# Performance work log

Measured on AMD Instinct MI355X. Metric: run time of the kernel, lower is better.

Reference implementation:

```python
import jax, jax.numpy as jnp
import numpy as np
from jax import lax

B, N, CIN, COUT, FPS, K, TCH, M, H = 8, 4096, 128, 256, 1024, 24, 256, 32, 4
HD = TCH // H
BN_SCALE = 1.0 / np.sqrt(1.0 + 1e-5)  # eval-mode BN: running_mean=0, running_var=1


def _gather(points, idx):
    # points [B,N,C], idx [B,S] or [B,S,K] -> gathered points
    return jax.vmap(lambda p, i: p[i])(points, idx)


def _bn(x, g, b):
    return x * (g * BN_SCALE) + b


def _ln(x, g, b):
    mu = jnp.mean(x, -1, keepdims=True)
    v = jnp.var(x, -1, keepdims=True)
    return (x - mu) / jnp.sqrt(v + 1e-5) * g + b


def _gelu(x):
    return jax.nn.gelu(x, approximate=False)


def _fps(xyz, npoint, farthest0):
    Bb, Nn, _ = xyz.shape
    def step(carry, _):
        dmin, far = carry
        c = jax.vmap(lambda p, i: p[i])(xyz, far)  # [B,3]
        d = jnp.sum((xyz - c[:, None, :]) ** 2, -1)
        dmin = jnp.minimum(dmin, d)
        return (dmin, jnp.argmax(dmin, -1)), far
    init = (jnp.full((Bb, Nn), 1e10, xyz.dtype), farthest0)
    _, cents = lax.scan(step, init, None, length=npoint)
    return cents.T  # [B, npoint]


def _sqdist(src, dst):
    d = -2.0 * jnp.einsum('bnc,bmc->bnm', src, dst)
    d = d + jnp.sum(src ** 2, -1)[:, :, None]
    d = d + jnp.sum(dst ** 2, -1)[:, None, :]
    return d


def _forward(xyz, x, t, farthest0, Wproj, gproj, bproj, Wl1, gl1, bl1, Wl2, gl2, bl2,
             Wc1, gc1, bc1, Wc2, gc2, bc2, Wq, Wk, Wv, Wo,
             ln1g, ln1b, Wqkv, Wao, ln2g, ln2b, Wf1, Wf2):
    # --- GenerateGraph: FPS + KNN grouping ---
    fps_idx = _fps(xyz, FPS, farthest0)            # [B,S]
    new_xyz = _gather(xyz, fps_idx)                # [B,S,3]
    xT = jnp.transpose(x, (0, 2, 1))               # [B,N,Cin]
    new_pts = _gather(xT, fps_idx)                 # [B,S,Cin]
    dist = _sqdist(new_xyz, xyz)                   # [B,S,N]
    _, idx = lax.top_k(-dist, K)                   # [B,S,K] nearest neighbors
    grouped = _gather(xT, idx)                     # [B,S,K,Cin]
    edge = grouped - new_pts[:, :, None, :]
    # --- Local: Conv1DBR proj + Conv1DBRRes (channels-last, 1x1 convs = GEMM) ---
    h = _gelu(_bn(jnp.einsum('bskc,oc->bsko', edge, Wproj), gproj, bproj))
    r = _gelu(_bn(jnp.einsum('bsko,po->bskp', h, Wl1), gl1, bl1))
    r = _bn(jnp.einsum('bskp,op->bsko', r, Wl2), gl2, bl2)
    h = _gelu(r + h)
    f = jnp.max(h, axis=2)                         # adaptive_max_pool over k -> [B,S,O]
    # --- Channel (ca): Conv1DBRRes on centroid features ---
    r = _gelu(_bn(f @ Wc1.T, gc1, bc1))
    r = _bn(r @ Wc2.T, gc2, bc2)
    f = _gelu(r + f)
    x_out = jnp.transpose(f, (0, 2, 1))            # [B,O,S]
    # --- Local2Former: tokens attend to local features ---
    q = t @ Wq.T
    kk = f @ Wk.T
    v = f @ Wv.T
    a = jax.nn.softmax(jnp.einsum('bmd,bsd->bms', q, kk) * (TCH ** -0.5), axis=-1)
    t = t + jnp.einsum('bms,bsd->bmd', a, v) @ Wo.T
    # --- Former: one pre-norm encoder layer (MHA + MLP) ---
    hn = _ln(t, ln1g, ln1b)
    qkv = (hn @ Wqkv.T).reshape(B, M, 3, H, HD).transpose(2, 0, 3, 1, 4)
    qh, kh, vh = qkv[0], qkv[1], qkv[2]            # [B,H,M,hd]
    attn = jax.nn.softmax(jnp.einsum('bhmd,bhnd->bhmn', qh, kh) * (HD ** -0.5), axis=-1)
    o = jnp.einsum('bhmn,bhnd->bhmd', attn, vh).transpose(0, 2, 1, 3).reshape(B, M, TCH)
    t = t + o @ Wao.T
    hn = _ln(t, ln2g, ln2b)
    t = t + _gelu(hn @ Wf1.T) @ Wf2.T
    return new_xyz, x_out, t


def setup_inputs() -> dict:
    key = jax.random.key(0)
    ks = jax.random.split(key, 40)
    def w(k, o, i):
        return jax.random.normal(k, (o, i), jnp.float32) / np.sqrt(i)
    def g(k, c):
        return 1.0 + 0.1 * jax.random.normal(k, (c,), jnp.float32)
    def bta(k, c):
        return 0.1 * jax.random.normal(k, (c,), jnp.float32)
    inp = {
        'xyz': jax.random.normal(ks[0], (B, N, 3), jnp.float32),
        'x': jax.random.normal(ks[1], (B, CIN, N), jnp.float32),
        't': jax.random.normal(ks[2], (B, M, TCH), jnp.float32),
        'farthest0': jax.random.randint(ks[3], (B,), 0, N),
        'Wproj': w(ks[4], COUT, CIN), 'gproj': g(ks[5], COUT), 'bproj': bta(ks[6], COUT),
        'Wl1': w(ks[7], COUT, COUT), 'gl1': g(ks[8], COUT), 'bl1': bta(ks[9], COUT),
        'Wl2': w(ks[10], COUT, COUT), 'gl2': g(ks[11], COUT), 'bl2': bta(ks[12], COUT),
        'Wc1': w(ks[13], COUT, COUT), 'gc1': g(ks[14], COUT), 'bc1': bta(ks[15], COUT),
        'Wc2': w(ks[16], COUT, COUT), 'gc2': g(ks[17], COUT), 'bc2': bta(ks[18], COUT),
        'Wq': w(ks[19], TCH, TCH), 'Wk': w(ks[20], TCH, COUT), 'Wv': w(ks[21], TCH, COUT),
        'Wo': w(ks[22], TCH, TCH),
        'ln1g': g(ks[23], TCH), 'ln1b': bta(ks[24], TCH),
        'Wqkv': w(ks[25], 3 * TCH, TCH), 'Wao': w(ks[26], TCH, TCH),
        'ln2g': g(ks[27], TCH), 'ln2b': bta(ks[28], TCH),
        'Wf1': w(ks[29], 2 * TCH, TCH), 'Wf2': w(ks[30], TCH, 2 * TCH),
    }
    return inp


def reference(xyz, x, t, farthest0, Wproj, gproj, bproj, Wl1, gl1, bl1, Wl2, gl2, bl2,
              Wc1, gc1, bc1, Wc2, gc2, bc2, Wq, Wk, Wv, Wo,
              ln1g, ln1b, Wqkv, Wao, ln2g, ln2b, Wf1, Wf2):
    return _forward(xyz, x, t, farthest0, Wproj, gproj, bproj, Wl1, gl1, bl1, Wl2, gl2, bl2,
                    Wc1, gc1, bc1, Wc2, gc2, bc2, Wq, Wk, Wv, Wo,
                    ln1g, ln1b, Wqkv, Wao, ln2g, ln2b, Wf1, Wf2)
```

## Files before the change

### kernel.cpp

```cpp
#include <hip/hip_runtime.h>
#include <math.h>

#define Bc 8
#define Nc 4096
#define CINc 128
#define COUTc 256
#define Sc 1024
#define Kc 24
#define TCHc 256
#define Mc 32
#define Hc 4
#define HDc 64
#define MBAT (Sc*Kc)

#define BN_SCALE_F 0.9999950000374997f

typedef __attribute__((ext_vector_type(8))) short bf16x8;
typedef __attribute__((ext_vector_type(4))) float f32x4;
typedef __attribute__((ext_vector_type(2))) float f32x2;

__device__ __forceinline__ float b2f(short s){
  unsigned int u = ((unsigned int)(unsigned short)s) << 16;
  union { unsigned int u; float f; } c; c.u = u; return c.f;
}
__device__ __forceinline__ short f2b(float f){
  union { unsigned int u; float f; } c; c.f = f;
  unsigned int u = c.u;
  unsigned int r = (u + 0x7fffu + ((u >> 16) & 1u)) >> 16;
  return (short)(r & 0xffffu);
}
__device__ __forceinline__ float gelu_f(float v){
  return 0.5f * v * (1.f + erff(v * 0.7071067811865475f));
}
__device__ __forceinline__ float rdval(const float* p){ return *p; }
__device__ __forceinline__ float rdval(const short* p){ return b2f(*p); }
__device__ __forceinline__ void wrval(float* p, float v){ *p = v; }
__device__ __forceinline__ void wrval(short* p, float v){ *p = f2b(v); }

__device__ __forceinline__ void gl_lds16(const short* g, short* l){
  __builtin_amdgcn_global_load_lds(
     (const __attribute__((address_space(1))) void*)g,
     (__attribute__((address_space(3))) void*)l, 16, 0, 0);
}

__device__ __forceinline__ void bar_lds(){
  asm volatile("s_waitcnt lgkmcnt(0)" ::: "memory");
  __builtin_amdgcn_s_barrier();
}

__device__ __forceinline__ f32x2 pk_add(f32x2 a, f32x2 b){
  f32x2 d; asm("v_pk_add_f32 %0, %1, %2" : "=v"(d) : "v"(a), "v"(b)); return d;
}
__device__ __forceinline__ f32x2 pk_mul(f32x2 a, f32x2 b){
  f32x2 d; asm("v_pk_mul_f32 %0, %1, %2" : "=v"(d) : "v"(a), "v"(b)); return d;
}

__device__ __forceinline__ double packkey(float d, unsigned tag){
  return __longlong_as_double((long long)(
    (((unsigned long long)(unsigned)__float_as_int(d)) << 32) | (unsigned long long)tag));
}

template<int CTRL>
__device__ __forceinline__ double dpp_mov_f64(double v){
  long long x = __double_as_longlong(v);
  int lo = (int)(unsigned)(x & 0xFFFFFFFFLL);
  int hi = (int)(unsigned)((unsigned long long)x >> 32);
  int plo = __builtin_amdgcn_update_dpp(lo, lo, CTRL, 0xF, 0xF, false);
  int phi = __builtin_amdgcn_update_dpp(hi, hi, CTRL, 0xF, 0xF, false);
  return __longlong_as_double((long long)(((unsigned long long)(unsigned)phi << 32)
                                          | (unsigned)plo));
}
template<int CTRL>
__device__ __forceinline__ double dpp_min_f64(double v){
  return fmin(v, dpp_mov_f64<CTRL>(v));
}
template<int CTRL>
__device__ __forceinline__ float dpp_max_f32(float v){
  int p = __builtin_amdgcn_update_dpp(__float_as_int(v), __float_as_int(v), CTRL, 0xF, 0xF, false);
  return fmaxf(v, __int_as_float(p));
}

#define PREP_FPS 8
#define PREP_TOTAL 256
#define NWORK 248

__global__ __launch_bounds__(512) void prep_kernel(
    const float* __restrict__ xyz, const int* __restrict__ far0, int* __restrict__ fps_idx,
    const float* __restrict__ x, short* __restrict__ xT,
    const float* __restrict__ Wproj, const float* __restrict__ Wl1, const float* __restrict__ Wl2,
    const float* __restrict__ Wc1, const float* __restrict__ Wc2,
    const float* __restrict__ Wk, const float* __restrict__ Wv,
    const float* __restrict__ Wq, const float* __restrict__ Wo,
    const float* __restrict__ Wqkv, const float* __restrict__ Wao,
    const float* __restrict__ Wf1, const float* __restrict__ Wf2,
    const float* __restrict__ t_in,
    short* __restrict__ wbf,
    int* __restrict__ knn_idx, float* __restrict__ out0){
  __shared__ __align__(16) char smemc[57728];
  int bid = blockIdx.x, tid = threadIdx.x;
  if(bid < PREP_FPS){
    int b = bid;
    float* sx = (float*)smemc;
    float* sy = sx + Nc;
    float* sz = sy + Nc;
    double* pwave = (double*)(smemc + 49152);
    const float* xb = xyz + (size_t)b*Nc*3;
    for(int i=tid; i<Nc; i+=512){
      const float* p = xb + i*3;
      sx[i]=p[0]; sy[i]=p[1]; sz[i]=p[2];
    }
    __syncthreads();
    int lane = tid & 63, wv = tid >> 6;
    int base = wv*512 + lane*8;
    f32x2 px2[4], py2[4], pz2[4];
    float dmn[8];
#pragma unroll
    for(int i=0;i<4;i++){
      px2[i] = (f32x2){ sx[base+2*i], sx[base+2*i+1] };
      py2[i] = (f32x2){ sy[base+2*i], sy[base+2*i+1] };
      pz2[i] = (f32x2){ sz[base+2*i], sz[base+2*i+1] };
      dmn[2*i] = 1e10f; dmn[2*i+1] = 1e10f;
    }
    int winner = far0[b] & (Nc-1);
    int* out = fps_idx + b*Sc;
    for(int it=0; it<Sc; it++){
      if(tid==0)
        __hip_atomic_store(&out[it], winner, __ATOMIC_RELAXED, __HIP_MEMORY_SCOPE_AGENT);
      float cx=sx[winner], cy=sy[winner], cz=sz[winner];
      f32x2 ncx = (f32x2){-cx,-cx}, ncy = (f32x2){-cy,-cy}, ncz = (f32x2){-cz,-cz};
      float vmax = -1.f;
#pragma unroll
      for(int i=0;i<4;i++){
        f32x2 dx = pk_add(px2[i], ncx);
        f32x2 dy = pk_add(py2[i], ncy);
        f32x2 dz = pk_add(pz2[i], ncz);
        f32x2 d  = pk_add(pk_add(pk_mul(dx,dx), pk_mul(dy,dy)), pk_mul(dz,dz));
        dmn[2*i]   = fminf(dmn[2*i],   d[0]);
        dmn[2*i+1] = fminf(dmn[2*i+1], d[1]);
        vmax = fmaxf(vmax, fmaxf(dmn[2*i], dmn[2*i+1]));
      }
      float wm = vmax;
      wm = dpp_max_f32<0x111>(wm);
      wm = dpp_max_f32<0x112>(wm);
      wm = dpp_max_f32<0x114>(wm);
      wm = dpp_max_f32<0x118>(wm);
      wm = dpp_max_f32<0x142>(wm);
      wm = dpp_max_f32<0x143>(wm);
      float smax = __int_as_float(__builtin_amdgcn_readlane(__float_as_int(wm), 63));
      int lj = 0;
#pragma unroll
      for(int j=7;j>=0;j--) if(dmn[j]==smax) lj = j;
      unsigned long long mk = __ballot(vmax == smax);
      int flane = __ffsll(mk) - 1;
      int ljw = __builtin_amdgcn_readlane(lj, flane);
      int widx = wv*512 + flane*8 + ljw;
      if(lane==0)
        pwave[(it&1)*8 + wv] = packkey(smax, (unsigned)((Nc-1) - widx));
      bar_lds();
      const double* pb = pwave + (it&1)*8;
      double kb = fmax(fmax(fmax(pb[0],pb[1]), fmax(pb[2],pb[3])),
                       fmax(fmax(pb[4],pb[5]), fmax(pb[6],pb[7])));
      winner = (Nc-1) - (int)(unsigned)(__double_as_longlong(kb) & 0xFFFFFFFFULL);
    }
  } else {
    int wid = bid - PREP_FPS;
    int b = wid / 31;
    int widb = wid % 31;
    short (*tile)[33] = (short(*)[33])smemc;
    for(int t = wid; t < 4096; t += NWORK){
      int bb = t >> 9;
      int rem = t & 511;
      int n0 = (rem & 127) * 32;
      int c0 = (rem >> 7) * 32;
      int tx = tid & 31, ty = tid >> 5;
      __syncthreads();
#pragma unroll
      for(int i=0;i<32;i+=16)
        tile[ty+i][tx] = f2b(x[((size_t)bb*CINc + (c0+ty+i))*Nc + n0+tx]);
      __syncthreads();
#pragma unroll
      for(int i=0;i<32;i+=16)
        xT[((size_t)bb*Nc + (n0+ty+i))*CINc + c0+tx] = tile[tx][ty+i];
    }
    {
      int gid = wid*512 + tid;
      const int stride = NWORK*512;
      short* p = wbf;
      for(int i=gid; i<COUTc*CINc; i+=stride) p[i] = f2b(Wproj[i]);
      p += COUTc*CINc;
      for(int i=gid; i<COUTc*COUTc; i+=stride) p[i] = f2b(Wl1[i]);
      p += COUTc*COUTc;
      for(int i=gid; i<COUTc*COUTc; i+=stride) p[i] = f2b(Wl2[i]);
      p += COUTc*COUTc;
      for(int i=gid; i<COUTc*COUTc; i+=stride) p[i] = f2b(Wc1[i]);
      p += COUTc*COUTc;
      for(int i=gid; i<COUTc*COUTc; i+=stride) p[i] = f2b(Wc2[i]);
      p += COUTc*COUTc;
      for(int i=gid; i<TCHc*COUTc; i+=stride) p[i] = f2b(Wk[i]);
      p += TCHc*COUTc;
      for(int i=gid; i<TCHc*COUTc; i+=stride) p[i] = f2b(Wv[i]);
      p += TCHc*COUTc;
      for(int i=gid; i<TCHc*TCHc; i+=stride) p[i] = f2b(Wq[i]);
      p += TCHc*TCHc;
      for(int i=gid; i<TCHc*TCHc; i+=stride) p[i] = f2b(Wo[i]);
      p += TCHc*TCHc;
      for(int i=gid; i<3*TCHc*TCHc; i+=stride) p[i] = f2b(Wqkv[i]);
      p += 3*TCHc*TCHc;
      for(int i=gid; i<TCHc*TCHc; i+=stride) p[i] = f2b(Wao[i]);
      p += TCHc*TCHc;
      for(int i=gid; i<2*TCHc*TCHc; i+=stride) p[i] = f2b(Wf1[i]);
      p += 2*TCHc*TCHc;
      for(int i=gid; i<2*TCHc*TCHc; i+=stride) p[i] = f2b(Wf2[i]);
      p += 2*TCHc*TCHc;
      for(int i=gid; i<Bc*Mc*TCHc; i+=stride) p[i] = f2b(t_in[i]);
    }
    int* s_qn = (int*)(smemc + 2112);
    double* pvd = (double*)(smemc + 2176);
    const float* xb = xyz + (size_t)b*Nc*3;
    float px[8], py[8], pz[8], db[8];
#pragma unroll
    for(int j=0;j<8;j++){
      int n = tid + 512*j;
      float xx=xb[n*3], yy=xb[n*3+1], zz=xb[n*3+2];
      px[j]=xx; py[j]=yy; pz[j]=zz;
      db[j] = __fadd_rn(__fadd_rn(__fmul_rn(xx,xx),__fmul_rn(yy,yy)),__fmul_rn(zz,zz));
    }
    __syncthreads();
    for(int s = widb; s < Sc; s += 31){
      if(tid==0){
        int qn;
        for(;;){
          qn = __hip_atomic_load(&fps_idx[b*Sc + s], __ATOMIC_RELAXED, __HIP_MEMORY_SCOPE_AGENT);
          if(qn >= 0) break;
          __builtin_amdgcn_s_sleep(8);
        }
        s_qn[0] = qn & (Nc-1);
      }
      bar_lds();
      int qn = s_qn[0];
      const float* q = xyz + ((size_t)b*Nc + qn)*3;
      float sxq = q[0], syq = q[1], szq = q[2];
      if(tid < 3) out0[((size_t)b*Sc + s)*3 + tid] = q[tid];
      float ss = __fadd_rn(__fadd_rn(__fmul_rn(sxq,sxq),__fmul_rn(syq,syq)),__fmul_rn(szq,szq));
      float dv[8];
#pragma unroll
      for(int j=0;j<8;j++){
        float e = __fmul_rn(sxq,px[j]);
        e = __fadd_rn(e, __fmul_rn(syq,py[j]));
        e = __fadd_rn(e, __fmul_rn(szq,pz[j]));
        dv[j] = __fadd_rn(__fadd_rn(__fmul_rn(-2.f,e), ss), db[j]);
      }
      int* ob = knn_idx + ((size_t)b*Sc + s)*Kc;
      for(int k=0;k<Kc;k++){
        double kk = packkey(fmaxf(dv[0],0.f), (unsigned)tid);
#pragma unroll
        for(int j=1;j<8;j++) kk = fmin(kk, packkey(fmaxf(dv[j],0.f), (unsigned)(tid + 512*j)));
        kk = dpp_min_f64<0x111>(kk);
        kk = dpp_min_f64<0x112>(kk);
        kk = dpp_min_f64<0x114>(kk);
        kk = dpp_min_f64<0x118>(kk);
        kk = dpp_min_f64<0x142>(kk);
        kk = dpp_min_f64<0x143>(kk);
        double* pb = pvd + (k&1)*8;
        if((tid&63)==63) pb[tid>>6] = kk;
        bar_lds();
        double w0 = fmin(fmin(fmin(pb[0],pb[1]),fmin(pb[2],pb[3])),
                         fmin(fmin(pb[4],pb[5]),fmin(pb[6],pb[7])));
        int win = (int)(unsigned)(__double_as_longlong(w0) & 0xFFFFFFFFULL);
        if(tid==0) ob[k] = win;
#pragma unroll
        for(int j=0;j<8;j++) if(tid + 512*j == win) dv[j] = 3.4e38f;
      }
    }
  }
}

template<int HAS_BN, int HAS_GELU, int HAS_RES, typename TRES>
__global__ __launch_bounds__(256) void gemm128(
    const short* __restrict__ A, const short* __restrict__ W,
    const float* __restrict__ g, const float* __restrict__ bias,
    const TRES* __restrict__ Res, short* __restrict__ Out,
    int Nn, int Kk){
  __shared__ short As[128*32];
  __shared__ short Bs[128*32];
  int bm = blockIdx.y*128, bn = blockIdx.x*128;
  int tid = threadIdx.x;
  int wave = tid>>6, lane = tid&63, quad = lane>>4, l16 = lane&15;
  int wr = (wave>>1)*64, wc = (wave&1)*64;
  f32x4 acc[4][4];
#pragma unroll
  for(int i=0;i<4;i++)
#pragma unroll
    for(int j=0;j<4;j++) acc[i][j] = (f32x4){0.f,0.f,0.f,0.f};
  int sr = tid>>2, scc = (tid&3)*8;
  const short* Ap = A + (size_t)(bm+sr)*Kk + scc;
  const short* Wp = W + (size_t)(bn+sr)*Kk + scc;
  for(int k0=0; k0<Kk; k0+=32){
    gl_lds16(Ap + k0,                    As + tid*8);
    gl_lds16(Ap + k0 + (size_t)64*Kk,    As + 2048 + tid*8);
    gl_lds16(Wp + k0,                    Bs + tid*8);
    gl_lds16(Wp + k0 + (size_t)64*Kk,    Bs + 2048 + tid*8);
    __syncthreads();
    bf16x8 af[4], bfr[4];
#pragma unroll
    for(int mt=0; mt<4; mt++) af[mt]  = *(const bf16x8*)&As[(wr+mt*16+l16)*32 + quad*8];
#pragma unroll
    for(int nt=0; nt<4; nt++) bfr[nt] = *(const bf16x8*)&Bs[(wc+nt*16+l16)*32 + quad*8];
#pragma unroll
    for(int mt=0; mt<4; mt++)
#pragma unroll
      for(int nt=0; nt<4; nt++)
        acc[mt][nt] = __builtin_amdgcn_mfma_f32_16x16x32_bf16(af[mt], bfr[nt], acc[mt][nt], 0, 0, 0);
    __syncthreads();
  }
#pragma unroll
  for(int nt=0; nt<4; nt++){
    int col = bn + wc + nt*16 + l16;
    float gs = 0.f, bs_ = 0.f;
    if(HAS_BN){ gs = g[col] * BN_SCALE_F; bs_ = bias[col]; }
#pragma unroll
    for(int mt=0; mt<4; mt++){
#pragma unroll
      for(int r2=0;r2<4;r2++){
        int row = bm + wr + mt*16 + quad*4 + r2;
        float v = acc[mt][nt][r2];
        if(HAS_BN) v = v*gs + bs_;
        if(HAS_RES) v += rdval(Res + (size_t)row*Nn + col);
        if(HAS_GELU) v = gelu_f(v);
        Out[(size_t)row*Nn + col] = f2b(v);
      }
    }
  }
}

__global__ __launch_bounds__(256) void proj128(
    const short* __restrict__ xT, const int* __restrict__ knn_idx, const int* __restrict__ fps_idx,
    const short* __restrict__ W, const float* __restrict__ g, const float* __restrict__ bias,
    short* __restrict__ Out, int R0){
  __shared__ short As[128*32];
  __shared__ short Bs[128*32];
  int bm = blockIdx.y*128, bn = blockIdx.x*128;
  int tid = threadIdx.x;
  int wave = tid>>6, lane = tid&63, quad = lane>>4, l16 = lane&15;
  int wr = (wave>>1)*64, wc = (wave&1)*64;
  f32x4 acc[4][4];
#pragma unroll
  for(int i=0;i<4;i++)
#pragma unroll
    for(int j=0;j<4;j++) acc[i][j] = (f32x4){0.f,0.f,0.f,0.f};
  int sr = tid>>2, scc = (tid&3)*8;
  int Rg0 = R0 + bm + sr, Rg1 = Rg0 + 64;
  int b0 = Rg0 / (Sc*Kc), b1 = Rg1 / (Sc*Kc);
  int nk0 = knn_idx[Rg0] & (Nc-1), nk1 = knn_idx[Rg1] & (Nc-1);
  int nc0 = fps_idx[Rg0 / Kc] & (Nc-1), nc1 = fps_idx[Rg1 / Kc] & (Nc-1);
  const short* pk0 = xT + ((size_t)b0*Nc + nk0)*CINc + scc;
  const short* pc0 = xT + ((size_t)b0*Nc + nc0)*CINc + scc;
  const short* pk1 = xT + ((size_t)b1*Nc + nk1)*CINc + scc;
  const short* pc1 = xT + ((size_t)b1*Nc + nc1)*CINc + scc;
  const short* Wp  = W + (size_t)(bn+sr)*CINc + scc;
  for(int k0=0; k0<CINc; k0+=32){
    gl_lds16(Wp + k0,                      Bs + tid*8);
    gl_lds16(Wp + k0 + (size_t)64*CINc,    Bs + 2048 + tid*8);
    bf16x8 vk = *(const bf16x8*)(pk0 + k0);
    bf16x8 vc = *(const bf16x8*)(pc0 + k0);
    bf16x8 e0, e1;
#pragma unroll
    for(int i=0;i<8;i++) e0[i] = f2b(__fsub_rn(b2f(vk[i]), b2f(vc[i])));
    vk = *(const bf16x8*)(pk1 + k0);
    vc = *(const bf16x8*)(pc1 + k0);
#pragma unroll
    for(int i=0;i<8;i++) e1[i] = f2b(__fsub_rn(b2f(vk[i]), b2f(vc[i])));
    *(bf16x8*)&As[tid*8] = e0;
    *(bf16x8*)&As[2048 + tid*8] = e1;
    __syncthreads();
    bf16x8 af[4], bfr[4];
#pragma unroll
    for(int mt=0; mt<4; mt++) af[mt]  = *(const bf16x8*)&As[(wr+mt*16+l16)*32 + quad*8];
#pragma unroll
    for(int nt=0; nt<4; nt++) bfr[nt] = *(const bf16x8*)&Bs[(wc+nt*16+l16)*32 + quad*8];
#pragma unroll
    for(int mt=0; mt<4; mt++)
#pragma unroll
      for(int nt=0; nt<4; nt++)
        acc[mt][nt] = __builtin_amdgcn_mfma_f32_16x16x32_bf16(af[mt], bfr[nt], acc[mt][nt], 0, 0, 0);
    __syncthreads();
  }
#pragma unroll
  for(int nt=0; nt<4; nt++){
    int col = bn + wc + nt*16 + l16;
    float gs = g[col] * BN_SCALE_F, bs_ = bias[col];
#pragma unroll
    for(int mt=0; mt<4; mt++){
#pragma unroll
      for(int r2=0;r2<4;r2++){
        int row = bm + wr + mt*16 + quad*4 + r2;
        float v = acc[mt][nt][r2]*gs + bs_;
        Out[(size_t)row*COUTc + col] = f2b(gelu_f(v));
      }
    }
  }
}

__global__ __launch_bounds__(192) void gemm_l2max(
    const short* __restrict__ A, const short* __restrict__ W,
    const float* __restrict__ g, const float* __restrict__ bias,
    const short* __restrict__ Hres, short* __restrict__ Fout, int R0){
  __shared__ short As[48*32];
  __shared__ short Bs[64*32];
  __shared__ float sm[48][65];
  int bm = blockIdx.y*48, bn = blockIdx.x*64;
  int tid = threadIdx.x;
  int wave = tid >> 6, lane = tid & 63, quad = lane >> 4, l16 = lane & 15;
  f32x4 acc[4];
#pragma unroll
  for(int i=0;i<4;i++) acc[i] = (f32x4){0.f,0.f,0.f,0.f};
  const short* Ap  = A + (size_t)(bm + (tid>>2))*COUTc + (tid&3)*8;
  const short* Wp  = W + (size_t)(bn + (tid>>2))*COUTc + (tid&3)*8;
  const short* Wp2 = W + (size_t)(bn + 48 + (lane>>2))*COUTc + (lane&3)*8;
  for(int k0=0; k0<COUTc; k0+=32){
    gl_lds16(Ap + k0, As + tid*8);
    gl_lds16(Wp + k0, Bs + tid*8);
    if(wave==0) gl_lds16(Wp2 + k0, Bs + 1536 + lane*8);
    __syncthreads();
    bf16x8 a = *(const bf16x8*)&As[(wave*16 + l16)*32 + quad*8];
#pragma unroll
    for(int ct=0; ct<4; ct++){
      bf16x8 bb = *(const bf16x8*)&Bs[(ct*16 + l16)*32 + quad*8];
      acc[ct] = __builtin_amdgcn_mfma_f32_16x16x32_bf16(a, bb, acc[ct], 0, 0, 0);
    }
    __syncthreads();
  }
#pragma unroll
  for(int ct=0; ct<4; ct++){
    int col = bn + ct*16 + l16;
    float gs = g[col] * BN_SCALE_F, bs_ = bias[col];
#pragma unroll
    for(int r2=0;r2<4;r2++){
      int rl = wave*16 + quad*4 + r2;
      float v = acc[ct][r2]*gs + bs_;
      v += b2f(Hres[(size_t)(bm+rl)*COUTc + col]);
      sm[rl][ct*16 + l16] = gelu_f(v);
    }
  }
  __syncthreads();
  if(tid < 128){
    int gl = tid >> 6, col = tid & 63;
    float mx = -3.4e38f;
#pragma unroll
    for(int kk=0; kk<Kc; kk++) mx = fmaxf(mx, sm[gl*Kc + kk][col]);
    int gg = R0/Kc + blockIdx.y*2 + gl;
    Fout[(size_t)gg*COUTc + bn + col] = f2b(mx);
  }
}

template<int HAS_BN, int HAS_GELU, int HAS_RES, typename TRES, typename TOUT>
__global__ __launch_bounds__(256) void gemm64d(
    const short* __restrict__ A, const short* __restrict__ W,
    const float* __restrict__ g, const float* __restrict__ bias,
    const TRES* __restrict__ Res, TOUT* __restrict__ Out,
    int Nn, int Kk){
  __shared__ short As[64*32];
  __shared__ short Bs[64*32];
  int bm = blockIdx.y*64, bn = blockIdx.x*64;
  int tid = threadIdx.x;
  int wave = tid >> 6, lane = tid & 63, quad = lane >> 4, l16 = lane & 15;
  f32x4 acc[4];
#pragma unroll
  for(int i=0;i<4;i++) acc[i] = (f32x4){0.f,0.f,0.f,0.f};
  const short* Ap = A + (size_t)(bm + (tid>>2))*Kk + (tid&3)*8;
  const short* Wp = W + (size_t)(bn + (tid>>2))*Kk + (tid&3)*8;
  for(int k0=0; k0<Kk; k0+=32){
    gl_lds16(Ap + k0, As + tid*8);
    gl_lds16(Wp + k0, Bs + tid*8);
    __syncthreads();
    bf16x8 a = *(const bf16x8*)&As[(wave*16 + l16)*32 + quad*8];
#pragma unroll
    for(int ct=0; ct<4; ct++){
      bf16x8 bb = *(const bf16x8*)&Bs[(ct*16 + l16)*32 + quad*8];
      acc[ct] = __builtin_amdgcn_mfma_f32_16x16x32_bf16(a, bb, acc[ct], 0, 0, 0);
    }
    __syncthreads();
  }
#pragma unroll
  for(int ct=0; ct<4; ct++){
    int col = bn + ct*16 + l16;
    float gs = 0.f, bs_ = 0.f;
    if(HAS_BN){ gs = g[col] * BN_SCALE_F; bs_ = bias[col]; }
#pragma unroll
    for(int r2=0;r2<4;r2++){
      int row = bm + wave*16 + quad*4 + r2;
      float v = acc[ct][r2];
      if(HAS_BN) v = v*gs + bs_;
      if(HAS_RES) v += rdval(Res + (size_t)row*Nn + col);
      if(HAS_GELU) v = gelu_f(v);
      wrval(Out + (size_t)row*Nn + col, v);
    }
  }
}

__global__ __launch_bounds__(256) void transpose_f(const short* __restrict__ f2, float* __restrict__ out1){
  __shared__ short tile[32][33];
  int b = blockIdx.z;
  int s0 = blockIdx.x*32, c0 = blockIdx.y*32;
  int tx = threadIdx.x & 31, ty = threadIdx.x >> 5;
#pragma unroll
  for(int i=0;i<32;i+=8)
    tile[ty+i][tx] = f2[((size_t)b*Sc + (s0+ty+i))*COUTc + c0+tx];
  __syncthreads();
#pragma unroll
  for(int i=0;i<32;i+=8)
    out1[((size_t)b*COUTc + (c0+ty+i))*Sc + s0+tx] = b2f(tile[tx][ty+i]);
}

__global__ __launch_bounds__(256) void l2f_attn(
    const short* __restrict__ qb, const short* __restrict__ kv,
    short* __restrict__ ao){
  int blk = blockIdx.x; int b = blk / Mc; int m = blk % Mc;
  int tid = threadIdx.x;
  __shared__ float qs[TCHc];
  __shared__ float aw[Sc];
  __shared__ float red[8];
  qs[tid] = b2f(qb[(size_t)(b*Mc+m)*TCHc + tid]);
  __syncthreads();
  float sc[4];
#pragma unroll
  for(int jj=0;jj<4;jj++){
    int j = tid + 256*jj;
    const short* kp = kv + ((size_t)b*Sc + j)*512;
    float a = 0.f;
    for(int c=0;c<TCHc;c+=8){
      bf16x8 v8 = *(const bf16x8*)(kp + c);
#pragma unroll
      for(int i=0;i<8;i++) a += b2f(v8[i]) * qs[c+i];
    }
    sc[jj] = a * 0.0625f;
  }
  float mx = fmaxf(fmaxf(sc[0],sc[1]), fmaxf(sc[2],sc[3]));
#pragma unroll
  for(int off=32; off>0; off>>=1) mx = fmaxf(mx, __shfl_xor(mx, off));
  if((tid&63)==0) red[tid>>6] = mx;
  __syncthreads();
  mx = fmaxf(fmaxf(red[0],red[1]), fmaxf(red[2],red[3]));
  float se = 0.f;
#pragma unroll
  for(int jj=0;jj<4;jj++){
    float e = expf(sc[jj] - mx);
    aw[tid + 256*jj] = e;
    se += e;
  }
#pragma unroll
  for(int off=32; off>0; off>>=1) se += __shfl_xor(se, off);
  if((tid&63)==0) red[4 + (tid>>6)] = se;
  __syncthreads();
  se = red[4]+red[5]+red[6]+red[7];
  float inv = 1.f/se;
#pragma unroll
  for(int jj=0;jj<4;jj++) aw[tid + 256*jj] *= inv;
  __syncthreads();
  float acc = 0.f;
  const short* vp = kv + (size_t)b*Sc*512 + 256 + tid;
  for(int j=0;j<Sc;j++) acc += aw[j] * b2f(vp[(size_t)j*512]);
  ao[(size_t)(b*Mc+m)*TCHc + tid] = f2b(acc);
}

__global__ __launch_bounds__(64) void former_attn(const short* __restrict__ qkv, short* __restrict__ oa){
  int blk = blockIdx.x;
  int m = blk % Mc; int bh = blk / Mc; int h = bh % Hc; int b = bh / Hc;
  int lane = threadIdx.x;
  __shared__ float qs[HDc];
  __shared__ float aw2[32];
  const short* base = qkv + (size_t)(b*Mc)*(3*TCHc);
  qs[lane] = b2f(base[(size_t)m*3*TCHc + h*HDc + lane]);
  __syncthreads();
  int j = lane & 31;
  const short* kp = base + (size_t)j*3*TCHc + TCHc + h*HDc;
  float s = 0.f;
  for(int d=0; d<HDc; d+=8){
    bf16x8 v8 = *(const bf16x8*)(kp + d);
#pragma unroll
    for(int i=0;i<8;i++) s += b2f(v8[i]) * qs[d+i];
  }
  s *= 0.125f;
  float mx = s;
#pragma unroll
  for(int off=16; off>0; off>>=1) mx = fmaxf(mx, __shfl_xor(mx, off, 32));
  float e = expf(s - mx);
  float se = e;
#pragma unroll
  for(int off=16; off>0; off>>=1) se += __shfl_xor(se, off, 32);
  if(lane < 32) aw2[lane] = e / se;
  __syncthreads();
  float acc = 0.f;
  const short* vp = base + 2*TCHc + h*HDc + lane;
  for(int jj=0; jj<32; jj++) acc += aw2[jj] * b2f(vp[(size_t)jj*3*TCHc]);
  oa[(size_t)(b*Mc+m)*TCHc + h*HDc + lane] = f2b(acc);
}

__global__ __launch_bounds__(64) void ln_kernel(const float* __restrict__ X, const float* __restrict__ g,
                                                const float* __restrict__ bb, short* __restrict__ O){
  int row = blockIdx.x, lane = threadIdx.x;
  const float* xp = X + (size_t)row*TCHc;
  float x[4];
#pragma unroll
  for(int j2=0;j2<4;j2++) x[j2] = xp[lane + 64*j2];
  float sm = x[0]+x[1]+x[2]+x[3];
#pragma unroll
  for(int off=32; off>0; off>>=1) sm += __shfl_xor(sm, off);
  float mu = sm * (1.f/256.f);
  float vs = 0.f;
#pragma unroll
  for(int j2=0;j2<4;j2++){ float d = x[j2]-mu; vs += d*d; }
#pragma unroll
  for(int off=32; off>0; off>>=1) vs += __shfl_xor(vs, off);
  float var = vs * (1.f/256.f);
  float rstd = 1.f / sqrtf(var + 1e-5f);
#pragma unroll
  for(int j2=0;j2<4;j2++){
    int c = lane + 64*j2;
    float o = (x[j2]-mu)*rstd*g[c] + bb[c];
    O[(size_t)row*TCHc + c] = f2b(o);
  }
}

extern "C" void kernel_launch(void* const* d_in, const int* in_sizes, int n_in,
                              void* d_out, int out_size, void* d_ws, size_t ws_size,
                              hipStream_t stream){
  const float* xyz  = (const float*)d_in[0];
  const float* x    = (const float*)d_in[1];
  const float* t_in = (const float*)d_in[2];
  const int*   far0 = (const int*)d_in[3];
  const float* Wproj=(const float*)d_in[4];  const float* gproj=(const float*)d_in[5];  const float* bproj=(const float*)d_in[6];
  const float* Wl1 = (const float*)d_in[7];  const float* gl1 = (const float*)d_in[8];  const float* bl1 = (const float*)d_in[9];
  const float* Wl2 = (const float*)d_in[10]; const float* gl2 = (const float*)d_in[11]; const float* bl2 = (const float*)d_in[12];
  const float* Wc1 = (const float*)d_in[13]; const float* gc1 = (const float*)d_in[14]; const float* bc1 = (const float*)d_in[15];
  const float* Wc2 = (const float*)d_in[16]; const float* gc2 = (const float*)d_in[17]; const float* bc2 = (const float*)d_in[18];
  const float* Wq  = (const float*)d_in[19]; const float* Wk  = (const float*)d_in[20]; const float* Wv  = (const float*)d_in[21];
  const float* Wo  = (const float*)d_in[22];
  const float* ln1g= (const float*)d_in[23]; const float* ln1b= (const float*)d_in[24];
  const float* Wqkv= (const float*)d_in[25]; const float* Wao = (const float*)d_in[26];
  const float* ln2g= (const float*)d_in[27]; const float* ln2b= (const float*)d_in[28];
  const float* Wf1 = (const float*)d_in[29]; const float* Wf2 = (const float*)d_in[30];

  char* wsb = (char*)d_ws;
  size_t off = 0;
  auto alloc = [&](size_t bytes)->void*{ void* p = wsb + off; off += (bytes + 255) & ~(size_t)255; return p; };
  int*   fps_i = (int*)alloc((size_t)Bc*Sc*4);
  int*   knn   = (int*)alloc((size_t)Bc*Sc*Kc*4);
  short* xT    = (short*)alloc((size_t)Bc*Nc*CINc*2);
  size_t wbf_elems = (size_t)COUTc*CINc + 4*(size_t)COUTc*COUTc + 2*(size_t)TCHc*COUTc
                   + 2*(size_t)TCHc*TCHc + 3*(size_t)TCHc*TCHc + (size_t)TCHc*TCHc
                   + 2*(size_t)TCHc*TCHc + 2*(size_t)TCHc*TCHc + (size_t)Bc*Mc*TCHc;
  short* wbf   = (short*)alloc(wbf_elems*2);
  short* fbuf  = (short*)alloc((size_t)Bc*Sc*COUTc*2);
  short* rcbuf = (short*)alloc((size_t)Bc*Sc*COUTc*2);
  short* f2buf = (short*)alloc((size_t)Bc*Sc*COUTc*2);
  short* kvbuf = (short*)alloc((size_t)Bc*Sc*512*2);
  short* qbuf  = (short*)alloc((size_t)Bc*Mc*TCHc*2);
  short* a1out = (short*)alloc((size_t)Bc*Mc*TCHc*2);
  float* t1buf = (float*)alloc((size_t)Bc*Mc*TCHc*4);
  short* hnbuf = (short*)alloc((size_t)Bc*Mc*TCHc*2);
  short* qkvb  = (short*)alloc((size_t)Bc*Mc*3*TCHc*2);
  short* a2out = (short*)alloc((size_t)Bc*Mc*TCHc*2);
  float* t2buf = (float*)alloc((size_t)Bc*Mc*TCHc*4);
  short* hn2buf= (short*)alloc((size_t)Bc*Mc*TCHc*2);
  short* g1buf = (short*)alloc((size_t)Bc*Mc*2*TCHc*2);
  size_t full_bytes  = (size_t)Bc*MBAT*COUTc*2;
  size_t batch_bytes = (size_t)MBAT*COUTc*2;
  bool batched = (off + 2*(full_bytes + 256) <= ws_size);
  short* hbuf = (short*)alloc(batched ? full_bytes : batch_bytes);
  short* rbuf = (short*)alloc(batched ? full_bytes : batch_bytes);
  if(off > ws_size) return;

  short* wproj_bf = wbf;
  short* wl1_bf   = wproj_bf + COUTc*CINc;
  short* wl2_bf   = wl1_bf + COUTc*COUTc;
  short* wc1_bf   = wl2_bf + COUTc*COUTc;
  short* wc2_bf   = wc1_bf + COUTc*COUTc;
  short* wkv_bf   = wc2_bf + COUTc*COUTc;
  short* wq_bf    = wkv_bf + 2*TCHc*COUTc;
  short* wo_bf    = wq_bf + TCHc*TCHc;
  short* wqkv_bf  = wo_bf + TCHc*TCHc;
  short* wao_bf   = wqkv_bf + 3*TCHc*TCHc;
  short* wf1_bf   = wao_bf + TCHc*TCHc;
  short* wf2_bf   = wf1_bf + 2*TCHc*TCHc;
  short* tbf      = wf2_bf + 2*TCHc*TCHc;

  float* out0 = (float*)d_out;
  float* out1 = out0 + (size_t)Bc*Sc*3;
  float* out2 = out1 + (size_t)Bc*COUTc*Sc;

  hipMemsetAsync(fps_i, 0xFF, (size_t)Bc*Sc*4, stream);
  prep_kernel<<<PREP_TOTAL, 512, 0, stream>>>(xyz, far0, fps_i, x, xT,
                                              Wproj, Wl1, Wl2, Wc1, Wc2, Wk, Wv,
                                              Wq, Wo, Wqkv, Wao, Wf1, Wf2, t_in,
                                              wbf, knn, out0);
  if(batched){
    proj128<<<dim3(COUTc/128, (Bc*MBAT)/128), 256, 0, stream>>>(xT, knn, fps_i, wproj_bf, gproj, bproj, hbuf, 0);
    gemm128<1,1,0,short><<<dim3(COUTc/128, (Bc*MBAT)/128), 256, 0, stream>>>(hbuf, wl1_bf, gl1, bl1, (const short*)nullptr, rbuf, COUTc, COUTc);
    gemm_l2max<<<dim3(COUTc/64, (Bc*MBAT)/48), 192, 0, stream>>>(rbuf, wl2_bf, gl2, bl2, hbuf, fbuf, 0);
  } else {
    for(int b=0; b<Bc; b++){
      proj128<<<dim3(COUTc/128, MBAT/128), 256, 0, stream>>>(xT, knn, fps_i, wproj_bf, gproj, bproj, hbuf, b*MBAT);
      gemm128<1,1,0,short><<<dim3(COUTc/128, MBAT/128), 256, 0, stream>>>(hbuf, wl1_bf, gl1, bl1, (const short*)nullptr, rbuf, COUTc, COUTc);
      gemm_l2max<<<dim3(COUTc/64, MBAT/48), 192, 0, stream>>>(rbuf, wl2_bf, gl2, bl2, hbuf, fbuf, b*MBAT);
    }
  }
  gemm64d<1,1,0,short,short><<<dim3(COUTc/64, (Bc*Sc)/64), 256, 0, stream>>>(fbuf, wc1_bf, gc1, bc1, (const short*)nullptr, rcbuf, COUTc, COUTc);
  gemm64d<1,1,1,short,short><<<dim3(COUTc/64, (Bc*Sc)/64), 256, 0, stream>>>(rcbuf, wc2_bf, gc2, bc2, fbuf, f2buf, COUTc, COUTc);
  transpose_f<<<dim3(Sc/32, COUTc/32, Bc), 256, 0, stream>>>(f2buf, out1);
  gemm64d<0,0,0,short,short><<<dim3(TCHc/64, (Bc*Mc)/64), 256, 0, stream>>>(tbf, wq_bf, nullptr, nullptr, (const short*)nullptr, qbuf, TCHc, TCHc);
  gemm64d<0,0,0,short,short><<<dim3(512/64, (Bc*Sc)/64), 256, 0, stream>>>(f2buf, wkv_bf, nullptr, nullptr, (const short*)nullptr, kvbuf, 512, COUTc);
  l2f_attn<<<Bc*Mc, 256, 0, stream>>>(qbuf, kvbuf, a1out);
  gemm64d<0,0,1,float,float><<<dim3(TCHc/64, (Bc*Mc)/64), 256, 0, stream>>>(a1out, wo_bf, nullptr, nullptr, t_in, t1buf, TCHc, TCHc);
  ln_kernel<<<Bc*Mc, 64, 0, stream>>>(t1buf, ln1g, ln1b, hnbuf);
  gemm64d<0,0,0,short,short><<<dim3((3*TCHc)/64, (Bc*Mc)/64), 256, 0, stream>>>(hnbuf, wqkv_bf, nullptr, nullptr, (const short*)nullptr, qkvb, 3*TCHc, TCHc);
  former_attn<<<Bc*Hc*Mc, 64, 0, stream>>>(qkvb, a2out);
  gemm64d<0,0,1,float,float><<<dim3(TCHc/64, (Bc*Mc)/64), 256, 0, stream>>>(a2out, wao_bf, nullptr, nullptr, t1buf, t2buf, TCHc, TCHc);
  ln_kernel<<<Bc*Mc, 64, 0, stream>>>(t2buf, ln2g, ln2b, hn2buf);
  gemm64d<0,1,0,short,short><<<dim3((2*TCHc)/64, (Bc*Mc)/64), 256, 0, stream>>>(hn2buf, wf1_bf, nullptr, nullptr, (const short*)nullptr, g1buf, 2*TCHc, TCHc);
  gemm64d<0,0,1,float,float><<<dim3(TCHc/64, (Bc*Mc)/64), 256, 0, stream>>>(g1buf, wf2_bf, nullptr, nullptr, t2buf, out2, TCHc, 2*TCHc);
}
```

Before: 1.257 ms.

## Speculatively pick two FPS centroids per iteration using top-2 reduction

The farthest-point-sampling loop now reduces the top-2 packed (distance, index) keys per wave and across waves, instead of only the maximum. If the runner-up's distance to the new winner is at least its current min-distance, the runner-up must be the next FPS pick, so two centroids are emitted from one barrier round. This aims to roughly halve the serial block-barrier iterations on the FPS critical path. In exchange each reduction carries double-width keys and two DPP reduction chains, and the exactness relies on matching rounding in the recomputed distance check.

```diff
diff --git a/kernel.cpp b/kernel.cpp
--- a/kernel.cpp
+++ b/kernel.cpp
@@ -75,9 +75,14 @@
   return fmin(v, dpp_mov_f64<CTRL>(v));
 }
 template<int CTRL>
-__device__ __forceinline__ float dpp_max_f32(float v){
-  int p = __builtin_amdgcn_update_dpp(__float_as_int(v), __float_as_int(v), CTRL, 0xF, 0xF, false);
-  return fmaxf(v, __int_as_float(p));
+__device__ __forceinline__ double dpp_max_f64(double v){
+  return fmax(v, dpp_mov_f64<CTRL>(v));
+}
+__device__ __forceinline__ double readlane_f64(double v, int l){
+  long long x = __double_as_longlong(v);
+  int lo = __builtin_amdgcn_readlane((int)(unsigned)(x & 0xFFFFFFFFLL), l);
+  int hi = __builtin_amdgcn_readlane((int)(unsigned)((unsigned long long)x >> 32), l);
+  return __longlong_as_double((long long)(((unsigned long long)(unsigned)hi << 32) | (unsigned)lo));
 }
 
 #define PREP_FPS 8
@@ -103,7 +108,7 @@
     float* sx = (float*)smemc;
     float* sy = sx + Nc;
     float* sz = sy + Nc;
-    double* pwave = (double*)(smemc + 49152);
+    double* pw = (double*)(smemc + 49152);
     const float* xb = xyz + (size_t)b*Nc*3;
     for(int i=tid; i<Nc; i+=512){
       const float* p = xb + i*3;
@@ -113,54 +118,110 @@
     int lane = tid & 63, wv = tid >> 6;
     int base = wv*512 + lane*8;
     f32x2 px2[4], py2[4], pz2[4];
-    float dmn[8];
+    float dmn[8]; unsigned lokey[8];
 #pragma unroll
     for(int i=0;i<4;i++){
       px2[i] = (f32x2){ sx[base+2*i], sx[base+2*i+1] };
       py2[i] = (f32x2){ sy[base+2*i], sy[base+2*i+1] };
       pz2[i] = (f32x2){ sz[base+2*i], sz[base+2*i+1] };
       dmn[2*i] = 1e10f; dmn[2*i+1] = 1e10f;
-    }
-    int winner = far0[b] & (Nc-1);
+      lokey[2*i]   = (unsigned)((Nc-1) - (base+2*i));
+      lokey[2*i+1] = (unsigned)((Nc-1) - (base+2*i+1));
+    }
     int* out = fps_idx + b*Sc;
-    for(int it=0; it<Sc; it++){
+    int w0 = far0[b] & (Nc-1);
+    if(tid==0)
+      __hip_atomic_store(&out[0], w0, __ATOMIC_RELAXED, __HIP_MEMORY_SCOPE_AGENT);
+    float c1x = sx[w0], c1y = sy[w0], c1z = sz[w0];
+    float c2x = 0.f, c2y = 0.f, c2z = 0.f;
+    bool two = false;
+    int it = 1, fr = 0;
+    while(it < Sc){
+      if(two){
+        f32x2 n1x={-c1x,-c1x}, n1y={-c1y,-c1y}, n1z={-c1z,-c1z};
+        f32x2 n2x={-c2x,-c2x}, n2y={-c2y,-c2y}, n2z={-c2z,-c2z};
+#pragma unroll
+        for(int i=0;i<4;i++){
+          f32x2 dx=pk_add(px2[i],n1x), dy=pk_add(py2[i],n1y), dz=pk_add(pz2[i],n1z);
+          f32x2 d1=pk_add(pk_add(pk_mul(dx,dx),pk_mul(dy,dy)),pk_mul(dz,dz));
+          f32x2 ex=pk_add(px2[i],n2x), ey=pk_add(py2[i],n2y), ez=pk_add(pz2[i],n2z);
+          f32x2 d2=pk_add(pk_add(pk_mul(ex,ex),pk_mul(ey,ey)),pk_mul(ez,ez));
+          dmn[2*i]   = fminf(fminf(dmn[2*i],   d1[0]), d2[0]);
+          dmn[2*i+1] = fminf(fminf(dmn[2*i+1], d1[1]), d2[1]);
+        }
+      } else {
+        f32x2 n1x={-c1x,-c1x}, n1y={-c1y,-c1y}, n1z={-c1z,-c1z};
+#pragma unroll
+        for(int i=0;i<4;i++){
+          f32x2 dx=pk_add(px2[i],n1x), dy=pk_add(py2[i],n1y), dz=pk_add(pz2[i],n1z);
+          f32x2 d1=pk_add(pk_add(pk_mul(dx,dx),pk_mul(dy,dy)),pk_mul(dz,dz));
+          dmn[2*i]   = fminf(dmn[2*i],   d1[0]);
+          dmn[2*i+1] = fminf(dmn[2*i+1], d1[1]);
+        }
+      }
+      double kk0=packkey(dmn[0],lokey[0]), kk1=packkey(dmn[1],lokey[1]);
+      double kk2=packkey(dmn[2],lokey[2]), kk3=packkey(dmn[3],lokey[3]);
+      double kk4=packkey(dmn[4],lokey[4]), kk5=packkey(dmn[5],lokey[5]);
+      double kk6=packkey(dmn[6],lokey[6]), kk7=packkey(dmn[7],lokey[7]);
+      double h0=fmax(kk0,kk1), l0=fmin(kk0,kk1);
+      double h1=fmax(kk2,kk3), l1=fmin(kk2,kk3);
+      double h2=fmax(kk4,kk5), l2=fmin(kk4,kk5);
+      double h3=fmax(kk6,kk7), l3=fmin(kk6,kk7);
+      double m1a=fmax(h0,h1), m2a=fmax(fmin(h0,h1), (h0>h1)?l0:l1);
+      double m1b=fmax(h2,h3), m2b=fmax(fmin(h2,h3), (h2>h3)?l2:l3);
+      double w1=fmax(m1a,m1b), w2=fmax(fmin(m1a,m1b), (m1a>m1b)?m2a:m2b);
+      double kw = w1;
+      kw = dpp_max_f64<0x111>(kw);
+      kw = dpp_max_f64<0x112>(kw);
+      kw = dpp_max_f64<0x114>(kw);
+      kw = dpp_max_f64<0x118>(kw);
+      kw = dpp_max_f64<0x142>(kw);
+      kw = dpp_max_f64<0x143>(kw);
+      double K1w = readlane_f64(kw, 63);
+      double km = (w1 == K1w) ? w2 : w1;
+      km = dpp_max_f64<0x111>(km);
+      km = dpp_max_f64<0x112>(km);
+      km = dpp_max_f64<0x114>(km);
+      km = dpp_max_f64<0x118>(km);
+      km = dpp_max_f64<0x142>(km);
+      km = dpp_max_f64<0x143>(km);
+      int p = fr & 1;
+      if(lane==63){
+        double* row = pw + p*16 + wv*2;
+        row[0] = kw;
+        row[1] = km;
+      }
+      bar_lds();
+      fr++;
+      const double* q = pw + p*16;
+      double q10=q[0], q20=q[1], q11=q[2], q21=q[3], q12=q[4], q22=q[5], q13=q[6], q23=q[7],
+             q14=q[8], q24=q[9], q15=q[10], q25=q[11], q16=q[12], q26=q[13], q17=q[14], q27=q[15];
+      double g1 = fmax(fmax(fmax(q10,q11),fmax(q12,q13)),fmax(fmax(q14,q15),fmax(q16,q17)));
+      double a0=(q10==g1)?q20:q10, a1=(q11==g1)?q21:q11;
+      double a2=(q12==g1)?q22:q12, a3=(q13==g1)?q23:q13;
+      double a4=(q14==g1)?q24:q14, a5=(q15==g1)?q25:q15;
+      double a6=(q16==g1)?q26:q16, a7=(q17==g1)?q27:q17;
+      double g2 = fmax(fmax(fmax(a0,a1),fmax(a2,a3)),fmax(fmax(a4,a5),fmax(a6,a7)));
+      int idx1 = (Nc-1) - (int)(unsigned)(__double_as_longlong(g1) & 0xFFFFFFFFULL);
+      int idx2 = (Nc-1) - (int)(unsigned)(__double_as_longlong(g2) & 0xFFFFFFFFULL);
       if(tid==0)
-        __hip_atomic_store(&out[it], winner, __ATOMIC_RELAXED, __HIP_MEMORY_SCOPE_AGENT);
-      float cx=sx[winner], cy=sy[winner], cz=sz[winner];
-      f32x2 ncx = (f32x2){-cx,-cx}, ncy = (f32x2){-cy,-cy}, ncz = (f32x2){-cz,-cz};
-      float vmax = -1.f;
-#pragma unroll
-      for(int i=0;i<4;i++){
-        f32x2 dx = pk_add(px2[i], ncx);
-        f32x2 dy = pk_add(py2[i], ncy);
-        f32x2 dz = pk_add(pz2[i], ncz);
-        f32x2 d  = pk_add(pk_add(pk_mul(dx,dx), pk_mul(dy,dy)), pk_mul(dz,dz));
-        dmn[2*i]   = fminf(dmn[2*i],   d[0]);
-        dmn[2*i+1] = fminf(dmn[2*i+1], d[1]);
-        vmax = fmaxf(vmax, fmaxf(dmn[2*i], dmn[2*i+1]));
+        __hip_atomic_store(&out[it], idx1, __ATOMIC_RELAXED, __HIP_MEMORY_SCOPE_AGENT);
+      it++;
+      float nx=sx[idx1], ny=sy[idx1], nz=sz[idx1];
+      float rx=sx[idx2], ry=sy[idx2], rz=sz[idx2];
+      c1x=nx; c1y=ny; c1z=nz;
+      float ddx=__fsub_rn(rx,nx), ddy=__fsub_rn(ry,ny), ddz=__fsub_rn(rz,nz);
+      float dd=__fadd_rn(__fadd_rn(__fmul_rn(ddx,ddx),__fmul_rn(ddy,ddy)),__fmul_rn(ddz,ddz));
+      unsigned tag2 = (unsigned)(__double_as_longlong(g2) & 0xFFFFFFFFULL);
+      double vk = packkey(dd, tag2);
+      if(it < Sc && vk >= g2){
+        if(tid==0)
+          __hip_atomic_store(&out[it], idx2, __ATOMIC_RELAXED, __HIP_MEMORY_SCOPE_AGENT);
+        it++;
+        two = true; c2x=rx; c2y=ry; c2z=rz;
+      } else {
+        two = false;
       }
-      float wm = vmax;
-      wm = dpp_max_f32<0x111>(wm);
-      wm = dpp_max_f32<0x112>(wm);
-      wm = dpp_max_f32<0x114>(wm);
-      wm = dpp_max_f32<0x118>(wm);
-      wm = dpp_max_f32<0x142>(wm);
-      wm = dpp_max_f32<0x143>(wm);
-      float smax = __int_as_float(__builtin_amdgcn_readlane(__float_as_int(wm), 63));
-      int lj = 0;
-#pragma unroll
-      for(int j=7;j>=0;j--) if(dmn[j]==smax) lj = j;
-      unsigned long long mk = __ballot(vmax == smax);
-      int flane = __ffsll(mk) - 1;
-      int ljw = __builtin_amdgcn_readlane(lj, flane);
-      int widx = wv*512 + flane*8 + ljw;
-      if(lane==0)
-        pwave[(it&1)*8 + wv] = packkey(smax, (unsigned)((Nc-1) - widx));
-      bar_lds();
-      const double* pb = pwave + (it&1)*8;
-      double kb = fmax(fmax(fmax(pb[0],pb[1]), fmax(pb[2],pb[3])),
-                       fmax(fmax(pb[4],pb[5]), fmax(pb[6],pb[7])));
-      winner = (Nc-1) - (int)(unsigned)(__double_as_longlong(kb) & 0xFFFFFFFFULL);
     }
   } else {
     int wid = bid - PREP_FPS;
```

Result: faster. 1.215 ms (-3.4%).
